# Performance work log

Hardware: AMD Instinct MI355X
Metric: run time of the kernel (lower is better)

The kernel has to match this reference:

```python
import jax, jax.numpy as jnp
import numpy as np

K = 9
INF = 1.0e10
EPS = 1e-8

def setup_inputs() -> dict:
    key = jax.random.key(0)
    k1, k2 = jax.random.split(key)
    x = jax.random.normal(k1, (32, 128, 32, 32), dtype=jnp.float32)
    W = jax.random.normal(k2, (128, 128, K), dtype=jnp.float32) * 0.02
    return {"x": x, "W": W}

def reference(x, W):
    # x: (B, C, H, Wd); W: (C_out, C_in, K) conv1d weight, no bias
    B, C, H, Wd = x.shape
    N = H * Wd
    xf = x.reshape(B, C, N)  # tokens along last dim

    # cosine similarity matrix over channel dim -> (B, N, N)
    xn = xf / (jnp.linalg.norm(xf, axis=1, keepdims=True) + EPS)
    sim = jnp.einsum('bcn,bcm->bnm', xn, xn)
    # self-similarity forced to +INF so each token is its own first neighbor
    diag = jnp.arange(N)
    sim = sim.at[:, diag, diag].set(INF)

    # top-K most similar neighbors (maximum=True for cosine)
    _, idx = jax.lax.top_k(sim, K)  # (B, N, K) int32

    # gather neighbor features: (B, C, N, K)
    prime = jax.vmap(lambda xb, ib: xb[:, ib])(xf, idx)

    # Conv1d(kernel=K, stride=K, padding=0, bias=False) over flattened (B, C, N*K)
    # == contraction over (C_in, K) per token
    out = jnp.einsum('bcnk,ock->bon', prime, W)  # (B, C_out, N)
    return out.reshape(B, W.shape[0], H, Wd)
```

## Files before the change

kernel.cpp:

```cpp
#include <hip/hip_runtime.h>
#include <hip/hip_bf16.h>

#define TPB 256
#define STPB 512

typedef float f32x4 __attribute__((ext_vector_type(4)));
typedef short s16x8 __attribute__((ext_vector_type(8)));

static constexpr int B_ = 32;
static constexpr int C_ = 128;
static constexpr int N_ = 1024;
static constexpr int K_ = 9;
static constexpr int CN_ = C_ * N_;
static constexpr float INFV = 1.0e10f;
static constexpr float EPS_ = 1e-8f;

static constexpr size_t XNT_OFF = 0;
static constexpr size_t XNB_OFF = (size_t)B_ * CN_;
static constexpr size_t WBH_OFF = XNB_OFF + (size_t)B_ * CN_ / 2;
static constexpr size_t WBL_OFF = WBH_OFF + (size_t)K_ * C_ * C_ / 2;
static constexpr size_t CI_OFF  = WBL_OFF + (size_t)K_ * C_ * C_ / 2;
static constexpr size_t IDX_OFF = CI_OFF + (size_t)B_ * N_ * 16;

__device__ __forceinline__ void gload_lds16(const void* g, void* l) {
    __builtin_amdgcn_global_load_lds((const __attribute__((address_space(1))) void*)g,
                                     (__attribute__((address_space(3))) void*)l, 16, 0, 0);
}

#define INSERT9(Vv, Ii, vexpr, gmexpr)                                      \
    {                                                                       \
        float _v = (vexpr); int _gm = (gmexpr);                             \
        bool bp[9];                                                         \
        _Pragma("unroll")                                                   \
        for (int _p = 0; _p < 9; ++_p)                                      \
            bp[_p] = (_v > Vv[_p]) || (_v == Vv[_p] && _gm < Ii[_p]);       \
        if (bp[8]) {                                                        \
            _Pragma("unroll")                                               \
            for (int _p = 8; _p >= 1; --_p) {                               \
                Vv[_p] = bp[_p - 1] ? Vv[_p - 1] : (bp[_p] ? _v  : Vv[_p]); \
                Ii[_p] = bp[_p - 1] ? Ii[_p - 1] : (bp[_p] ? _gm : Ii[_p]); \
            }                                                               \
            if (bp[0]) { Vv[0] = _v; Ii[0] = _gm; }                         \
        }                                                                   \
    }

#define KINSERT(KEYS, THR, KEXPR)                                           \
    {                                                                       \
        unsigned _k = (KEXPR);                                              \
        if (_k > (THR)) {                                                   \
            _Pragma("unroll")                                               \
            for (int _p = 0; _p < 16; ++_p)                                 \
                KEYS[_p] = (KEYS[_p] == (THR)) ? _k : KEYS[_p];             \
            unsigned _a0 = min(KEYS[0],  KEYS[1]);                          \
            unsigned _a1 = min(KEYS[2],  KEYS[3]);                          \
            unsigned _a2 = min(KEYS[4],  KEYS[5]);                          \
            unsigned _a3 = min(KEYS[6],  KEYS[7]);                          \
            unsigned _a4 = min(KEYS[8],  KEYS[9]);                          \
            unsigned _a5 = min(KEYS[10], KEYS[11]);                         \
            unsigned _a6 = min(KEYS[12], KEYS[13]);                         \
            unsigned _a7 = min(KEYS[14], KEYS[15]);                         \
            _a0 = min(_a0, _a1); _a2 = min(_a2, _a3);                       \
            _a4 = min(_a4, _a5); _a6 = min(_a6, _a7);                       \
            _a0 = min(_a0, _a2); _a4 = min(_a4, _a6);                       \
            (THR) = min(_a0, _a4);                                          \
        }                                                                   \
    }

__device__ __forceinline__ unsigned simkey(float v, unsigned lowfield) {
    unsigned u = __float_as_uint(v);
    u ^= ((unsigned)((int)u >> 31) | 0x80000000u);
    return (u & 0xFFFFFC00u) | lowfield;
}

__global__ __launch_bounds__(TPB) void normtrans_kernel(const float* __restrict__ x,
                                                        float* __restrict__ xnt,
                                                        __hip_bfloat16* __restrict__ xnb) {
    __shared__ float lds[128][65];
    __shared__ float nrm[64];
    int b = blockIdx.x >> 4, n0 = (blockIdx.x & 15) << 6;
    const float* src = x + (size_t)b * CN_ + n0;
    #pragma unroll 4
    for (int i = 0; i < 32; ++i) {
        int flat = i * TPB + threadIdx.x;
        int c = flat >> 6, nn = flat & 63;
        lds[c][nn] = src[(size_t)c * N_ + nn];
    }
    __syncthreads();
    if (threadIdx.x < 64) {
        float ss = 0.f;
        #pragma unroll 8
        for (int c = 0; c < C_; ++c) { float v = lds[c][threadIdx.x]; ss += v * v; }
        nrm[threadIdx.x] = sqrtf(ss) + EPS_;
    }
    __syncthreads();
    float* dstf = xnt + ((size_t)b * N_ + n0) * C_;
    __hip_bfloat16* dstb = xnb + ((size_t)b * N_ + n0) * C_;
    #pragma unroll 4
    for (int i = 0; i < 32; ++i) {
        int flat = i * TPB + threadIdx.x;
        int nn = flat >> 7, c = flat & 127;
        float v = lds[c][nn] / nrm[nn];
        dstf[(size_t)nn * C_ + c] = v;
        dstb[(size_t)nn * C_ + c] = __float2bfloat16(v);
    }
}

__global__ __launch_bounds__(TPB) void transpose_bf16_kernel(const float* __restrict__ x,
                                                             __hip_bfloat16* __restrict__ xtb) {
    __shared__ float lds[128][65];
    int b = blockIdx.x >> 4, n0 = (blockIdx.x & 15) << 6;
    const float* src = x + (size_t)b * CN_ + n0;
    #pragma unroll 4
    for (int i = 0; i < 32; ++i) {
        int flat = i * TPB + threadIdx.x;
        int c = flat >> 6, nn = flat & 63;
        lds[c][nn] = src[(size_t)c * N_ + nn];
    }
    __syncthreads();
    __hip_bfloat16* dst = xtb + (size_t)b * CN_ + (size_t)n0 * C_;
    #pragma unroll 4
    for (int i = 0; i < 32; ++i) {
        int flat = i * TPB + threadIdx.x;
        int nn = flat >> 7, c = flat & 127;
        dst[(size_t)nn * C_ + c] = __float2bfloat16(lds[c][nn]);
    }
}

__global__ __launch_bounds__(TPB) void wbprep_kernel(const float* __restrict__ W,
                                                     __hip_bfloat16* __restrict__ wh,
                                                     __hip_bfloat16* __restrict__ wl) {
    int t = blockIdx.x * TPB + threadIdx.x;
    int k = t / (C_ * C_);
    int r = t - k * (C_ * C_);
    int o = r >> 7, c = r & 127;
    float w = W[((size_t)o * C_ + c) * K_ + k];
    __hip_bfloat16 h = __float2bfloat16(w);
    wh[t] = h;
    wl[t] = __float2bfloat16(w - __bfloat162float(h));
}

__global__ __launch_bounds__(STPB, 1) void sim_mfma_topk_kernel(const __hip_bfloat16* __restrict__ xnb,
                                                                int* __restrict__ ci) {
    __shared__ __align__(16) __hip_bfloat16 Ab[2][128 * 64];
    __shared__ __align__(16) __hip_bfloat16 Bb[2][128 * 64];
    __shared__ __align__(16) float scanb[128 * 132];

    const int tid = threadIdx.x;
    const int lane = tid & 63;
    const int wv = tid >> 6;
    const int b  = blockIdx.x >> 3;
    const int n0 = (blockIdx.x & 7) << 7;
    const __hip_bfloat16* xb = xnb + (size_t)b * CN_;
    const int l15 = lane & 15, l7 = lane & 7, lq = lane >> 4;
    const int swz = ((lane & 7) ^ (lane >> 3)) * 8;
    const int srow = tid & 127;
    const int sseg = tid >> 7;
    const int grow = n0 + srow;

#define STAGE_HALF(DST, TB, HH)                                            \
    {                                                                      \
        _Pragma("unroll")                                                  \
        for (int p_ = 0; p_ < 2; ++p_) {                                   \
            int r0_ = 16 * wv + 8 * p_;                                    \
            int tok_ = (TB) + r0_ + (lane >> 3);                           \
            gload_lds16(xb + (size_t)tok_ * C_ + (HH) * 64 + swz,          \
                        (DST) + r0_ * 64);                                 \
        }                                                                  \
    }

    STAGE_HALF(&Ab[0][0], n0, 0)
    STAGE_HALF(&Ab[1][0], n0, 1)
    STAGE_HALF(&Bb[0][0], 0, 0)
    STAGE_HALF(&Bb[1][0], 0, 1)
    __syncthreads();

    s16x8 af[2][2];
    #pragma unroll
    for (int h = 0; h < 2; ++h)
        #pragma unroll
        for (int kc = 0; kc < 2; ++kc)
            af[h][kc] = *(const s16x8*)&Ab[h][(16 * wv + l15) * 64 + (((kc * 4 + lq) ^ l7) << 3)];

    unsigned keys[16];
    #pragma unroll
    for (int p = 0; p < 16; ++p) keys[p] = (unsigned)p;
    unsigned thr = 0u;

    #pragma unroll 1
    for (int mt = 0; mt < 8; ++mt) {
        const int m0 = mt << 7;
        f32x4 acc[8];
        #pragma unroll
        for (int nt = 0; nt < 8; ++nt) acc[nt] = (f32x4){0.f, 0.f, 0.f, 0.f};

        #pragma unroll
        for (int h = 0; h < 2; ++h)
            #pragma unroll
            for (int kc = 0; kc < 2; ++kc) {
                const int phys = ((kc * 4 + lq) ^ l7) << 3;
                #pragma unroll
                for (int nt = 0; nt < 8; ++nt) {
                    s16x8 bb = *(const s16x8*)&Bb[h][(16 * nt + l15) * 64 + phys];
                    acc[nt] = __builtin_amdgcn_mfma_f32_16x16x32_bf16(af[h][kc], bb, acc[nt], 0, 0, 0);
                }
            }
        __syncthreads();

        if (mt < 7) {
            STAGE_HALF(&Bb[0][0], m0 + 128, 0)
            STAGE_HALF(&Bb[1][0], m0 + 128, 1)
        }
        #pragma unroll
        for (int nt = 0; nt < 8; ++nt)
            #pragma unroll
            for (int r = 0; r < 4; ++r)
                scanb[(16 * wv + 4 * lq + r) * 132 + 16 * nt + l15] = acc[nt][r];
        __syncthreads();

        const float* sp = &scanb[srow * 132 + (sseg << 5)];
        const int cb = m0 + (sseg << 5);
        const unsigned gb = 1023u - (unsigned)cb;
        const int drel = grow - cb;
        #pragma unroll 1
        for (int q = 0; q < 8; ++q) {
            float4 v4 = *(const float4*)(sp + 4 * q);
            float vv[4] = {v4.x, v4.y, v4.z, v4.w};
            #pragma unroll
            for (int j = 0; j < 4; ++j) {
                float v = (4 * q + j == drel) ? INFV : vv[j];
                KINSERT(keys, thr, simkey(v, gb - (unsigned)(4 * q + j)))
            }
        }
    }

    __syncthreads();
    unsigned* fk = (unsigned*)scanb;
    if (sseg) {
        int base = (srow * 3 + (sseg - 1)) * 16;
        #pragma unroll
        for (int p = 0; p < 16; ++p)
            fk[base + ((p + srow) & 15)] = keys[p];
    }
    __syncthreads();
    if (tid < 128) {
        #pragma unroll 1
        for (int g = 0; g < 3; ++g)
            #pragma unroll
            for (int p = 0; p < 16; ++p) {
                unsigned k = fk[(tid * 3 + g) * 16 + ((p + tid) & 15)];
                KINSERT(keys, thr, k)
            }
        int* op = ci + ((size_t)b * N_ + grow) * 16;
        #pragma unroll
        for (int p = 0; p < 16; ++p) op[p] = 1023 - (int)(keys[p] & 1023u);
    }
#undef STAGE_HALF
}

__global__ __launch_bounds__(TPB) void rescore_kernel(const float* __restrict__ xnt,
                                                      const int* __restrict__ ci,
                                                      int* __restrict__ idxo) {
    const int tid = threadIdx.x;
    const int g = tid >> 4, l = tid & 15;
    const size_t row = (size_t)blockIdx.x * 16 + g;
    const int nrow = (int)(row & (N_ - 1));
    const float* xbase = xnt + (row >> 10) * (size_t)CN_;
    const float* rvp = xbase + (size_t)nrow * C_;

    float rv[8];
    #pragma unroll
    for (int t = 0; t < 8; ++t) rv[t] = rvp[t * 16 + l];

    float val[9]; int id[9];
    #pragma unroll
    for (int p = 0; p < 9; ++p) { val[p] = -1e30f; id[p] = -1; }

    const int* cp = ci + row * 16;
    #pragma unroll 1
    for (int j = 0; j < 16; ++j) {
        int cand = cp[j];
        const float* cv = xbase + (size_t)cand * C_;
        float s = 0.f;
        #pragma unroll
        for (int t = 0; t < 8; ++t) s = fmaf(rv[t], cv[t * 16 + l], s);
        #pragma unroll
        for (int d = 1; d < 16; d <<= 1) s += __shfl_xor(s, d);
        float v = (cand == nrow) ? INFV : s;
        INSERT9(val, id, v, cand)
    }
    if (l == 0) {
        int* op = idxo + row * 9;
        #pragma unroll
        for (int p = 0; p < 9; ++p) op[p] = id[p];
    }
}

__global__ __launch_bounds__(TPB) void conv_mfma_kernel(const __hip_bfloat16* __restrict__ xtb,
                                                        const __hip_bfloat16* __restrict__ wbh,
                                                        const __hip_bfloat16* __restrict__ wbl,
                                                        const int* __restrict__ idxi,
                                                        float* __restrict__ out) {
    __shared__ __align__(16) __hip_bfloat16 gbuf[2][128 * 64];
    __shared__ __align__(16) __hip_bfloat16 hbuf[2][128 * 64];
    __shared__ __align__(16) __hip_bfloat16 lbuf[2][128 * 64];
    __shared__ int ids[K_ * 128];

    const int tid = threadIdx.x;
    const int lane = tid & 63;
    const int wv = tid >> 6;
    const int b  = blockIdx.x >> 3;
    const int n0 = (blockIdx.x & 7) << 7;
    const __hip_bfloat16* xb = xtb + (size_t)b * CN_;

    for (int j = tid; j < K_ * 128; j += TPB) {
        int k = j >> 7, r = j & 127;
        ids[j] = idxi[((size_t)b * N_ + n0 + r) * K_ + k];
    }
    __syncthreads();

    f32x4 acc[2][8];
    #pragma unroll
    for (int mt = 0; mt < 2; ++mt)
        #pragma unroll
        for (int nt = 0; nt < 8; ++nt) acc[mt][nt] = (f32x4){0.f, 0.f, 0.f, 0.f};

    const int swz = ((lane & 7) ^ (lane >> 3)) * 8;

#define CONV_STAGE(S, PB)                                                               \
    {                                                                                   \
        const int k_ = (S) >> 1, ch_ = ((S) & 1) * 64;                                  \
        _Pragma("unroll")                                                               \
        for (int q_ = 0; q_ < 4; ++q_) {                                                \
            int row_ = 32 * wv + 8 * q_ + (lane >> 3);                                  \
            int tok_ = ids[k_ * 128 + row_];                                            \
            gload_lds16(xb + (size_t)tok_ * C_ + ch_ + swz, &gbuf[PB][(32 * wv + 8 * q_) * 64]); \
            const size_t wr_ = ((size_t)k_ * 128 + row_) * C_ + ch_ + swz;              \
            gload_lds16(wbh + wr_, &hbuf[PB][(32 * wv + 8 * q_) * 64]);                 \
            gload_lds16(wbl + wr_, &lbuf[PB][(32 * wv + 8 * q_) * 64]);                 \
        }                                                                               \
    }

    CONV_STAGE(0, 0)
    __syncthreads();

    const int l15 = lane & 15, l7 = lane & 7, lq = lane >> 4;
    int pb = 0;
    #pragma unroll 1
    for (int s = 0; s < 18; ++s) {
        if (s < 17) CONV_STAGE(s + 1, pb ^ 1)
        const __hip_bfloat16* G = gbuf[pb];
        const __hip_bfloat16* H = hbuf[pb];
        const __hip_bfloat16* L = lbuf[pb];
        #pragma unroll
        for (int kc = 0; kc < 2; ++kc) {
            const int phys = ((kc * 4 + lq) ^ l7) * 8;
            s16x8 bb[8];
            #pragma unroll
            for (int nt = 0; nt < 8; ++nt)
                bb[nt] = *(const s16x8*)&G[(16 * nt + l15) * 64 + phys];
            #pragma unroll
            for (int mt = 0; mt < 2; ++mt) {
                const int orow = (32 * wv + 16 * mt + l15) * 64 + phys;
                s16x8 ah = *(const s16x8*)&H[orow];
                s16x8 al = *(const s16x8*)&L[orow];
                #pragma unroll
                for (int nt = 0; nt < 8; ++nt) {
                    acc[mt][nt] = __builtin_amdgcn_mfma_f32_16x16x32_bf16(ah, bb[nt], acc[mt][nt], 0, 0, 0);
                    acc[mt][nt] = __builtin_amdgcn_mfma_f32_16x16x32_bf16(al, bb[nt], acc[mt][nt], 0, 0, 0);
                }
            }
        }
        __syncthreads();
        pb ^= 1;
    }

    float* ob = out + (size_t)b * CN_;
    #pragma unroll
    for (int mt = 0; mt < 2; ++mt)
        #pragma unroll
        for (int nt = 0; nt < 8; ++nt) {
            int o = 32 * wv + 16 * mt + lq * 4;
            int n = n0 + 16 * nt + l15;
            #pragma unroll
            for (int r = 0; r < 4; ++r)
                ob[(size_t)(o + r) * N_ + n] = acc[mt][nt][r];
        }
#undef CONV_STAGE
}

extern "C" void kernel_launch(void* const* d_in, const int* in_sizes, int n_in,
                              void* d_out, int out_size, void* d_ws, size_t ws_size,
                              hipStream_t stream) {
    (void)in_sizes; (void)n_in; (void)out_size; (void)ws_size;
    const float* x = (const float*)d_in[0];
    const float* W = (const float*)d_in[1];
    float* out = (float*)d_out;
    float* ws  = (float*)d_ws;

    float* xnt = ws + XNT_OFF;
    __hip_bfloat16* xnb = (__hip_bfloat16*)(ws + XNB_OFF);
    __hip_bfloat16* xtb = (__hip_bfloat16*)(ws + XNB_OFF);
    __hip_bfloat16* wbh = (__hip_bfloat16*)(ws + WBH_OFF);
    __hip_bfloat16* wbl = (__hip_bfloat16*)(ws + WBL_OFF);
    int* ci  = (int*)(ws + CI_OFF);
    int* idx = (int*)(ws + IDX_OFF);

    normtrans_kernel<<<B_ * 16, TPB, 0, stream>>>(x, xnt, xnb);
    wbprep_kernel<<<(K_ * C_ * C_) / TPB, TPB, 0, stream>>>(W, wbh, wbl);
    sim_mfma_topk_kernel<<<B_ * 8, STPB, 0, stream>>>(xnb, ci);
    rescore_kernel<<<(B_ * N_) / 16, TPB, 0, stream>>>(xnt, ci, idx);
    transpose_bf16_kernel<<<B_ * 16, TPB, 0, stream>>>(x, xtb);
    conv_mfma_kernel<<<B_ * 8, TPB, 0, stream>>>(xtb, wbh, wbl, idx, out);
}
```

Before: 161.3 us.

## Restructure sim top-k kernel to select in registers with shuffle-based merge

The similarity/top-k kernel now handles 64 rows per block, using 16 blocks per batch. Each wave computes a 64-column slice with swapped MFMA operands, so every lane holds scores for a single row and inserts them into its top-16 straight from the accumulators. This removes the LDS score staging buffer and its extra barriers, and cuts shared memory enough to allow two blocks per CU. Partial lists are merged with cross-lane shuffles and one small LDS exchange. Four lanes per row now each run redundant insertion work, and the rescore loop unroll is also raised.

Measured after the change: 157.7 us. 2.2% less time.

```diff
diff --git a/kernel.cpp b/kernel.cpp
--- a/kernel.cpp
+++ b/kernel.cpp
@@ -139,39 +139,38 @@
     wl[t] = __float2bfloat16(w - __bfloat162float(h));
 }
 
-__global__ __launch_bounds__(STPB, 1) void sim_mfma_topk_kernel(const __hip_bfloat16* __restrict__ xnb,
+__global__ __launch_bounds__(STPB, 2) void sim_mfma_topk_kernel(const __hip_bfloat16* __restrict__ xnb,
                                                                 int* __restrict__ ci) {
-    __shared__ __align__(16) __hip_bfloat16 Ab[2][128 * 64];
-    __shared__ __align__(16) __hip_bfloat16 Bb[2][128 * 64];
-    __shared__ __align__(16) float scanb[128 * 132];
+    __shared__ __align__(16) ushort SH[8192 + 16384];
+    ushort* Ab = SH;
+    ushort* Bb = SH + 8192;
 
     const int tid = threadIdx.x;
     const int lane = tid & 63;
     const int wv = tid >> 6;
-    const int b  = blockIdx.x >> 3;
-    const int n0 = (blockIdx.x & 7) << 7;
+    const int rb = wv & 3;
+    const int ch = wv >> 2;
+    const int b  = blockIdx.x >> 4;
+    const int n0 = (blockIdx.x & 15) << 6;
     const __hip_bfloat16* xb = xnb + (size_t)b * CN_;
     const int l15 = lane & 15, l7 = lane & 7, lq = lane >> 4;
     const int swz = ((lane & 7) ^ (lane >> 3)) * 8;
-    const int srow = tid & 127;
-    const int sseg = tid >> 7;
-    const int grow = n0 + srow;
-
-#define STAGE_HALF(DST, TB, HH)                                            \
-    {                                                                      \
-        _Pragma("unroll")                                                  \
-        for (int p_ = 0; p_ < 2; ++p_) {                                   \
-            int r0_ = 16 * wv + 8 * p_;                                    \
-            int tok_ = (TB) + r0_ + (lane >> 3);                           \
-            gload_lds16(xb + (size_t)tok_ * C_ + (HH) * 64 + swz,          \
-                        (DST) + r0_ * 64);                                 \
-        }                                                                  \
-    }
-
-    STAGE_HALF(&Ab[0][0], n0, 0)
-    STAGE_HALF(&Ab[1][0], n0, 1)
-    STAGE_HALF(&Bb[0][0], 0, 0)
-    STAGE_HALF(&Bb[1][0], 0, 1)
+    const int grow = n0 + 16 * rb + l15;
+
+    #pragma unroll
+    for (int q = 0; q < 2; ++q) {
+        int u = 2 * wv + q;
+        int hh = u >> 3, r0 = (u & 7) * 8;
+        gload_lds16(xb + (size_t)(n0 + r0 + (lane >> 3)) * C_ + hh * 64 + swz,
+                    Ab + hh * 4096 + r0 * 64);
+    }
+    #pragma unroll
+    for (int q = 0; q < 4; ++q) {
+        int u = 4 * wv + q;
+        int hh = u >> 4, r0 = (u & 15) * 8;
+        gload_lds16(xb + (size_t)(r0 + (lane >> 3)) * C_ + hh * 64 + swz,
+                    Bb + hh * 8192 + r0 * 64);
+    }
     __syncthreads();
 
     s16x8 af[2][2];
@@ -179,7 +178,7 @@
     for (int h = 0; h < 2; ++h)
         #pragma unroll
         for (int kc = 0; kc < 2; ++kc)
-            af[h][kc] = *(const s16x8*)&Ab[h][(16 * wv + l15) * 64 + (((kc * 4 + lq) ^ l7) << 3)];
+            af[h][kc] = *(const s16x8*)&Ab[h * 4096 + (16 * rb + l15) * 64 + (((kc * 4 + lq) ^ l7) << 3)];
 
     unsigned keys[16];
     #pragma unroll
@@ -188,10 +187,9 @@
 
     #pragma unroll 1
     for (int mt = 0; mt < 8; ++mt) {
-        const int m0 = mt << 7;
-        f32x4 acc[8];
-        #pragma unroll
-        for (int nt = 0; nt < 8; ++nt) acc[nt] = (f32x4){0.f, 0.f, 0.f, 0.f};
+        f32x4 acc[4];
+        #pragma unroll
+        for (int t = 0; t < 4; ++t) acc[t] = (f32x4){0.f, 0.f, 0.f, 0.f};
 
         #pragma unroll
         for (int h = 0; h < 2; ++h)
@@ -199,62 +197,59 @@
             for (int kc = 0; kc < 2; ++kc) {
                 const int phys = ((kc * 4 + lq) ^ l7) << 3;
                 #pragma unroll
-                for (int nt = 0; nt < 8; ++nt) {
-                    s16x8 bb = *(const s16x8*)&Bb[h][(16 * nt + l15) * 64 + phys];
-                    acc[nt] = __builtin_amdgcn_mfma_f32_16x16x32_bf16(af[h][kc], bb, acc[nt], 0, 0, 0);
+                for (int t = 0; t < 4; ++t) {
+                    s16x8 bb = *(const s16x8*)&Bb[h * 8192 + (64 * ch + 16 * t + l15) * 64 + phys];
+                    acc[t] = __builtin_amdgcn_mfma_f32_16x16x32_bf16(bb, af[h][kc], acc[t], 0, 0, 0);
                 }
             }
         __syncthreads();
 
         if (mt < 7) {
-            STAGE_HALF(&Bb[0][0], m0 + 128, 0)
-            STAGE_HALF(&Bb[1][0], m0 + 128, 1)
-        }
-        #pragma unroll
-        for (int nt = 0; nt < 8; ++nt)
-            #pragma unroll
-            for (int r = 0; r < 4; ++r)
-                scanb[(16 * wv + 4 * lq + r) * 132 + 16 * nt + l15] = acc[nt][r];
-        __syncthreads();
-
-        const float* sp = &scanb[srow * 132 + (sseg << 5)];
-        const int cb = m0 + (sseg << 5);
-        const unsigned gb = 1023u - (unsigned)cb;
-        const int drel = grow - cb;
-        #pragma unroll 1
-        for (int q = 0; q < 8; ++q) {
-            float4 v4 = *(const float4*)(sp + 4 * q);
-            float vv[4] = {v4.x, v4.y, v4.z, v4.w};
-            #pragma unroll
-            for (int j = 0; j < 4; ++j) {
-                float v = (4 * q + j == drel) ? INFV : vv[j];
-                KINSERT(keys, thr, simkey(v, gb - (unsigned)(4 * q + j)))
+            #pragma unroll
+            for (int q = 0; q < 4; ++q) {
+                int u = 4 * wv + q;
+                int hh = u >> 4, r0 = (u & 15) * 8;
+                gload_lds16(xb + (size_t)(128 * (mt + 1) + r0 + (lane >> 3)) * C_ + hh * 64 + swz,
+                            Bb + hh * 8192 + r0 * 64);
             }
         }
-    }
-
-    __syncthreads();
-    unsigned* fk = (unsigned*)scanb;
-    if (sseg) {
-        int base = (srow * 3 + (sseg - 1)) * 16;
+
+        const int colb = (mt << 7) + 64 * ch + 4 * lq;
+        #pragma unroll
+        for (int t = 0; t < 4; ++t)
+            #pragma unroll
+            for (int r = 0; r < 4; ++r) {
+                int gcol = colb + 16 * t + r;
+                float v = acc[t][r];
+                if (gcol == grow) v = INFV;
+                KINSERT(keys, thr, simkey(v, 1023u - (unsigned)gcol))
+            }
+        __syncthreads();
+    }
+
+    #pragma unroll
+    for (int d = 16; d <= 32; d <<= 1) {
+        unsigned inc[16];
         #pragma unroll
         for (int p = 0; p < 16; ++p)
-            fk[base + ((p + srow) & 15)] = keys[p];
-    }
-    __syncthreads();
-    if (tid < 128) {
-        #pragma unroll 1
-        for (int g = 0; g < 3; ++g)
-            #pragma unroll
-            for (int p = 0; p < 16; ++p) {
-                unsigned k = fk[(tid * 3 + g) * 16 + ((p + tid) & 15)];
-                KINSERT(keys, thr, k)
-            }
+            inc[p] = (unsigned)__shfl_xor((int)keys[p], d);
+        #pragma unroll
+        for (int p = 0; p < 16; ++p) KINSERT(keys, thr, inc[p])
+    }
+
+    unsigned* mbuf = (unsigned*)SH;
+    if (ch == 1 && lq == 0) {
+        #pragma unroll
+        for (int p = 0; p < 16; ++p) mbuf[(16 * rb + l15) * 16 + p] = keys[p];
+    }
+    __syncthreads();
+    if (ch == 0 && lq == 0) {
+        #pragma unroll
+        for (int p = 0; p < 16; ++p) KINSERT(keys, thr, mbuf[(16 * rb + l15) * 16 + p])
         int* op = ci + ((size_t)b * N_ + grow) * 16;
         #pragma unroll
         for (int p = 0; p < 16; ++p) op[p] = 1023 - (int)(keys[p] & 1023u);
     }
-#undef STAGE_HALF
 }
 
 __global__ __launch_bounds__(TPB) void rescore_kernel(const float* __restrict__ xnt,
@@ -276,7 +271,7 @@
     for (int p = 0; p < 9; ++p) { val[p] = -1e30f; id[p] = -1; }
 
     const int* cp = ci + row * 16;
-    #pragma unroll 1
+    #pragma unroll 4
     for (int j = 0; j < 16; ++j) {
         int cand = cp[j];
         const float* cv = xbase + (size_t)cand * C_;
@@ -407,7 +402,7 @@
 
     normtrans_kernel<<<B_ * 16, TPB, 0, stream>>>(x, xnt, xnb);
     wbprep_kernel<<<(K_ * C_ * C_) / TPB, TPB, 0, stream>>>(W, wbh, wbl);
-    sim_mfma_topk_kernel<<<B_ * 8, STPB, 0, stream>>>(xnb, ci);
+    sim_mfma_topk_kernel<<<B_ * 16, STPB, 0, stream>>>(xnb, ci);
     rescore_kernel<<<(B_ * N_) / 16, TPB, 0, stream>>>(xnt, ci, idx);
     transpose_bf16_kernel<<<B_ * 16, TPB, 0, stream>>>(x, xtb);
     conv_mfma_kernel<<<B_ * 8, TPB, 0, stream>>>(xtb, wbh, wbl, idx, out);
```
